# Kernel optimization log

Measured on AMD Instinct MI355X. Metric: run time of the kernel, lower is better.

Reference implementation:

```python
import jax, jax.numpy as jnp
import numpy as np

B, S, D, H, HD = 2, 1024, 1024, 16, 64
CKV, CQ, R, DFF, L, V = 256, 384, 32, 2816, 4, 32000
EPS = 1.1920929e-07  # torch RMSNorm default eps = finfo(float32).eps


def rmsnorm(x, w):
    return x * jax.lax.rsqrt(jnp.mean(x * x, -1, keepdims=True) + EPS) * w


def rope(x, base=10000.0):
    # x: [B, H, S, d]; GPT-NeoX style rotate-half, matches RoPE._neg_half
    d, s = x.shape[-1], x.shape[2]
    theta = 1.0 / base ** (jnp.arange(0, d, 2, dtype=jnp.float32) / d)
    ang = jnp.arange(s, dtype=jnp.float32)[:, None] * theta[None, :]
    ang = jnp.concatenate([ang, ang], -1)  # [s, d]
    neg = jnp.concatenate([-x[..., d // 2:], x[..., :d // 2]], -1)
    return x * jnp.cos(ang) + neg * jnp.sin(ang)


def forward(tokens, embed, w_kv_down, b_kv_down, w_q_down, b_q_down, w_kv_up, b_kv_up,
            w_q_up, b_q_up, w_o, b_o, kv_norm_w, q_norm_w, norm1_w, norm2_w,
            w_in, b_in, w_out, b_out, norm_f_w, w_head, b_head):
    h = embed[tokens]                                  # [B, S, D]
    causal = jnp.triu(jnp.ones((S, S), bool), 1)       # True above diagonal -> masked
    scale = np.float32(1.0 / np.sqrt(HD + R))
    for i in range(L):
        xn = rmsnorm(h, norm1_w[i])
        ckv = xn @ w_kv_down[i] + b_kv_down[i]         # [B, S, CKV+R]
        c_kv, k_rope = ckv[..., :CKV], ckv[..., CKV:]
        kv = rmsnorm(c_kv, kv_norm_w[i]) @ w_kv_up[i] + b_kv_up[i]
        kv = kv.reshape(B, S, H, 2 * HD).transpose(0, 2, 1, 3)  # [B, H, S, 2*HD]
        k, v = kv[..., :HD], kv[..., HD:]
        qf = rmsnorm(xn @ w_q_down[i] + b_q_down[i], q_norm_w[i]) @ w_q_up[i] + b_q_up[i]
        qf = qf.reshape(B, S, H, HD + R).transpose(0, 2, 1, 3)   # [B, H, S, HD+R]
        q, q_rope = qf[..., :HD], qf[..., HD:]
        k_rope = rope(k_rope[:, None, :, :])           # [B, 1, S, R], shared across heads
        q_rope = rope(q_rope)
        k = jnp.concatenate([k, jnp.broadcast_to(k_rope, (B, H, S, R))], -1)
        q = jnp.concatenate([q, q_rope], -1)
        a = jnp.einsum('bhqd,bhkd->bhqk', q, k) * scale
        a = jax.nn.softmax(jnp.where(causal, -jnp.inf, a), -1)
        attn = jnp.einsum('bhqk,bhkd->bhqd', a, v).transpose(0, 2, 1, 3).reshape(B, S, D)
        h = h + attn @ w_o[i] + b_o[i]
        uv = rmsnorm(h, norm2_w[i]) @ w_in[i] + b_in[i]  # [B, S, 2*DFF]
        h = h + (uv[..., :DFF] * jax.nn.silu(uv[..., DFF:])) @ w_out[i] + b_out[i]
    return rmsnorm(h, norm_f_w) @ w_head + b_head        # [B, S, V]


def setup_inputs() -> dict:
    key = jax.random.key(0)
    it = iter(jax.random.split(key, 24))
    w = lambda shp: jax.random.normal(next(it), shp, jnp.float32) * 0.02
    return dict(
        tokens=jax.random.randint(next(it), (B, S), 0, V),
        embed=w((V, D)),
        w_kv_down=w((L, D, CKV + R)), b_kv_down=w((L, CKV + R)),
        w_q_down=w((L, D, CQ)), b_q_down=w((L, CQ)),
        w_kv_up=w((L, CKV, 2 * HD * H)), b_kv_up=w((L, 2 * HD * H)),
        w_q_up=w((L, CQ, (HD + R) * H)), b_q_up=w((L, (HD + R) * H)),
        w_o=w((L, D, D)), b_o=w((L, D)),
        kv_norm_w=jnp.ones((L, CKV)), q_norm_w=jnp.ones((L, CQ)),
        norm1_w=jnp.ones((L, D)), norm2_w=jnp.ones((L, D)),
        w_in=w((L, D, 2 * DFF)), b_in=w((L, 2 * DFF)),
        w_out=w((L, DFF, D)), b_out=w((L, D)),
        norm_f_w=jnp.ones((D,)),
        w_head=w((D, V)), b_head=w((V,)),
    )


def reference(tokens, embed, w_kv_down, b_kv_down, w_q_down, b_q_down, w_kv_up, b_kv_up,
              w_q_up, b_q_up, w_o, b_o, kv_norm_w, q_norm_w, norm1_w, norm2_w,
              w_in, b_in, w_out, b_out, norm_f_w, w_head, b_head):
    return forward(tokens, embed, w_kv_down, b_kv_down, w_q_down, b_q_down, w_kv_up,
                   b_kv_up, w_q_up, b_q_up, w_o, b_o, kv_norm_w, q_norm_w, norm1_w,
                   norm2_w, w_in, b_in, w_out, b_out, norm_f_w, w_head, b_head)
```

## Files before the change

kernel.cpp:

```cpp
#include <hip/hip_runtime.h>
#include <cstdint>
#include <cstddef>

typedef unsigned short u16;
typedef __attribute__((__ext_vector_type__(8))) __bf16 bf16x8;
typedef __attribute__((__ext_vector_type__(4))) float f32x4;
typedef __attribute__((__ext_vector_type__(8))) unsigned short u16x8;

#define DEVI __device__ __forceinline__

constexpr int Bb = 2, Ss = 1024, Dd = 1024, Hh = 16;
constexpr int Mm = Bb * Ss;
constexpr int QKD = 128;
constexpr float EPSF = 1.1920929e-07f;
constexpr float NEG = -1e30f;
constexpr float QSCALE = 0.10206207261596577f;
constexpr float LOG1E4_16 = 9.210340371976184f / 16.f;

DEVI u16 f2b(float f) {
  union { float f; uint32_t u; } a; a.f = f;
  uint32_t r = a.u + 0x7FFFu + ((a.u >> 16) & 1u);
  return (u16)(r >> 16);
}
DEVI float b2f(u16 h) {
  union { uint32_t u; float f; } a; a.u = ((uint32_t)h) << 16; return a.f;
}

struct WJob { const float* src; u16* dst; long src_lstride; int K; int N; int perm; int ntiles; };
struct WJobs { WJob j[7]; };

__global__ __launch_bounds__(256) void k_wcvt_batch(WJobs jobs, int njobs,
                                                    int tiles_per_layer, long dst_lstride) {
  int bt = blockIdx.x;
  int layer = bt / tiles_per_layer;
  int t = bt - layer * tiles_per_layer;
  int ji = 0;
  while (ji < njobs - 1 && t >= jobs.j[ji].ntiles) { t -= jobs.j[ji].ntiles; ++ji; }
  const float* __restrict__ src = jobs.j[ji].src + (size_t)layer * jobs.j[ji].src_lstride;
  u16* __restrict__ dst = jobs.j[ji].dst + (size_t)layer * dst_lstride;
  const int K = jobs.j[ji].K, N = jobs.j[ji].N, perm = jobs.j[ji].perm;
  const int ktiles = K >> 6;
  const int bk = (t % ktiles) * 64;
  const int bn = (t / ktiles) * 64;
  __shared__ float ts[64][65];
  const int tid = threadIdx.x;
  {
    int c4 = tid & 15, r = tid >> 4;
    #pragma unroll
    for (int p = 0; p < 4; ++p) {
      int row = r + p * 16;
      int col = bn + c4 * 4;
      float4 v = make_float4(0.f, 0.f, 0.f, 0.f);
      if (col < N) v = *(const float4*)(src + (size_t)(bk + row) * N + col);
      ts[row][c4 * 4 + 0] = v.x; ts[row][c4 * 4 + 1] = v.y;
      ts[row][c4 * 4 + 2] = v.z; ts[row][c4 * 4 + 3] = v.w;
    }
  }
  __syncthreads();
  {
    int k8 = tid & 7, c = tid >> 3;
    #pragma unroll
    for (int p = 0; p < 2; ++p) {
      int cc = c + p * 32;
      int gcol = bn + cc;
      int row = perm ? ((gcol < 2816) ? (gcol * 2) : ((gcol - 2816) * 2 + 1)) : gcol;
      u16x8 o;
      #pragma unroll
      for (int q = 0; q < 8; ++q) o[q] = f2b(ts[k8 * 8 + q][cc]);
      *(u16x8*)(dst + (size_t)row * K + bk + k8 * 8) = o;
    }
  }
}

__global__ void k_embed(const int* __restrict__ tok, const float* __restrict__ emb,
                        float* __restrict__ h) {
  int m = blockIdx.x;
  int t = tok[m];
  const float4* src = (const float4*)(emb + (size_t)t * Dd);
  float4* dst = (float4*)(h + (size_t)m * Dd);
  dst[threadIdx.x] = src[threadIdx.x];
}

__global__ void k_rms(const float* __restrict__ in, int inStride,
                      const float* __restrict__ w, u16* __restrict__ out, int K) {
  int m = blockIdx.x;
  const float* x = in + (size_t)m * inStride;
  float ss = 0.f;
  for (int i = threadIdx.x; i < K; i += 256) { float v = x[i]; ss += v * v; }
  #pragma unroll
  for (int off = 32; off; off >>= 1) ss += __shfl_xor(ss, off);
  __shared__ float red[4];
  if ((threadIdx.x & 63) == 0) red[threadIdx.x >> 6] = ss;
  __syncthreads();
  float r = rsqrtf((red[0] + red[1] + red[2] + red[3]) / (float)K + EPSF);
  for (int i = threadIdx.x; i < K; i += 256)
    out[(size_t)m * K + i] = f2b(x[i] * r * w[i]);
}

__global__ void k_rms2(const float* __restrict__ in, const float* __restrict__ w1,
                       const float* __restrict__ w2, u16* __restrict__ out1,
                       u16* __restrict__ out2) {
  int m = blockIdx.x;
  const float* x = in + (size_t)m * 768;
  int tid = threadIdx.x;
  __shared__ float red[4];
  {
    float v = x[tid];
    float ss = v * v;
    #pragma unroll
    for (int off = 32; off; off >>= 1) ss += __shfl_xor(ss, off);
    if ((tid & 63) == 0) red[tid >> 6] = ss;
    __syncthreads();
    float r = rsqrtf((red[0] + red[1] + red[2] + red[3]) / 256.f + EPSF);
    out1[(size_t)m * 256 + tid] = f2b(v * r * w1[tid]);
    __syncthreads();
  }
  {
    float v0 = x[384 + tid];
    float v1 = (tid < 128) ? x[640 + tid] : 0.f;
    float ss = v0 * v0 + v1 * v1;
    #pragma unroll
    for (int off = 32; off; off >>= 1) ss += __shfl_xor(ss, off);
    if ((tid & 63) == 0) red[tid >> 6] = ss;
    __syncthreads();
    float r = rsqrtf((red[0] + red[1] + red[2] + red[3]) / 384.f + EPSF);
    out2[(size_t)m * 384 + tid] = f2b(v0 * r * w2[tid]);
    if (tid < 128) out2[(size_t)m * 384 + 256 + tid] = f2b(v1 * r * w2[256 + tid]);
  }
}

__global__ void k_buildkv(const u16* __restrict__ kv, const float* __restrict__ ckvq,
                          u16* __restrict__ Kb, u16* __restrict__ Vt) {
  int bh = blockIdx.x, chunk = blockIdx.y, role = blockIdx.z;
  int b = bh >> 4, h = bh & 15;
  if (role < 2) {
    __shared__ u16 t[32][33];
    int tx = threadIdx.x & 31, ty = threadIdx.x >> 5;
    int s0 = chunk * 32, d0 = role * 32;
    #pragma unroll
    for (int i = ty; i < 32; i += 8)
      t[i][tx] = kv[(size_t)(b * Ss + s0 + i) * 2048 + h * 128 + 64 + d0 + tx];
    __syncthreads();
    #pragma unroll
    for (int i = ty; i < 32; i += 8)
      Vt[((size_t)bh * 64 + d0 + i) * Ss + s0 + tx] = t[tx][i];
  } else {
    int idx = threadIdx.x;
    int d = idx & 127, r0 = idx >> 7;
    #pragma unroll
    for (int it = 0; it < 16; ++it) {
      int s = chunk * 32 + it * 2 + r0;
      int m = b * Ss + s;
      u16 kvv = 0;
      if (d < 64) kvv = kv[(size_t)m * 2048 + h * 128 + d];
      else if (d < 96) {
        int j = d - 64;
        float theta = __expf(-(float)(j & 15) * LOG1E4_16);
        float sn, cs;
        __sincosf((float)s * theta, &sn, &cs);
        const float* rr = ckvq + (size_t)m * 768 + 256;
        float x = rr[j], o = rr[j ^ 16];
        kvv = f2b(x * cs + ((j < 16) ? -o : o) * sn);
      }
      Kb[((size_t)bh * Ss + s) * QKD + d] = kvv;
    }
  }
}

#define GAS __attribute__((address_space(1)))
#define LAS __attribute__((address_space(3)))
DEVI void gll16(const void* g, void* l) {
  __builtin_amdgcn_global_load_lds((GAS const void*)g, (LAS void*)l, 16, 0, 0);
}
#define VMW(n) asm volatile("s_waitcnt vmcnt(" #n ")" ::: "memory")
#define FENCE asm volatile("" ::: "memory")

__global__ __launch_bounds__(256) void k_flash(
    const u16* __restrict__ qf, const u16* __restrict__ Kg,
    const u16* __restrict__ Vtg, u16* __restrict__ attn) {
  __shared__ u16 lK[2][64 * 128];
  __shared__ u16 lV[2][64 * 64];
  __shared__ u16 lP[4][16 * 64];
  const int tid = threadIdx.x;
  const int pair = blockIdx.x, bh = blockIdx.y;
  const int b = bh >> 4, h = bh & 15;
  const int lane = tid & 63, w = tid >> 6;
  const int g = lane >> 4, fr = lane & 15;
  const u16* Kh = Kg + (size_t)bh * Ss * QKD;
  const u16* Vh = Vtg + (size_t)bh * 64 * Ss;

  auto stageKV = [&](int buf, int kt) {
    int r = tid >> 4, c = tid & 15;
    #pragma unroll
    for (int gg = 0; gg < 4; ++gg) {
      int row = gg * 16 + r;
      const u16* src = Kh + (size_t)(kt * 64 + row) * QKD + ((c ^ (row & 7)) * 8);
      gll16(src, (u16*)lK[buf] + gg * 2048 + tid * 8);
    }
    int r2 = tid >> 3, c2 = tid & 7;
    #pragma unroll
    for (int gg = 0; gg < 2; ++gg) {
      int d = gg * 32 + r2;
      const u16* src = Vh + (size_t)d * Ss + kt * 64 + ((c2 ^ (d & 7)) * 8);
      gll16(src, (u16*)lV[buf] + gg * 2048 + tid * 8);
    }
  };

  for (int pass = 0; pass < 2; ++pass) {
    const int qt = pass ? (15 - pair) : pair;
    const int q0 = qt * 64;
    const int s_row = q0 + w * 16 + fr;
    const u16* qrow = qf + (size_t)(b * Ss + s_row) * 1536 + h * 96;
    bf16x8 af[4];
    {
      u16x8 r0 = *(const u16x8*)(qrow + g * 8);
      u16x8 r1 = *(const u16x8*)(qrow + 32 + g * 8);
      u16x8 r2 = *(const u16x8*)(qrow + 64 + g * 8);
      u16x8 a0, a1, a2, a3;
      #pragma unroll
      for (int q = 0; q < 8; ++q) {
        a0[q] = f2b(b2f(r0[q]) * QSCALE);
        a1[q] = f2b(b2f(r1[q]) * QSCALE);
        float x = b2f(r2[q]);
        float oth = __shfl_xor(x, 32);
        int jj = (g & 1) * 8 + q;
        float theta = __expf(-(float)jj * LOG1E4_16);
        float sn, cs;
        __sincosf((float)s_row * theta, &sn, &cs);
        float v = x * cs + ((g < 2) ? -oth : oth) * sn;
        a2[q] = f2b(v * QSCALE);
        a3[q] = 0;
      }
      af[0] = *(bf16x8*)&a0; af[1] = *(bf16x8*)&a1;
      af[2] = *(bf16x8*)&a2; af[3] = *(bf16x8*)&a3;
    }

    f32x4 acc_o[4] = {};
    float mrow = NEG, lrow = 0.f;

    stageKV(0, 0);

    for (int kt = 0; kt <= qt; ++kt) {
      const int cur = kt & 1;
      if (kt < qt) { stageKV(cur ^ 1, kt + 1); VMW(6); }
      else { VMW(0); }
      __builtin_amdgcn_s_barrier();
      FENCE;

      f32x4 accs[4] = {};
      #pragma unroll
      for (int j = 0; j < 4; ++j) {
        #pragma unroll
        for (int k4 = 0; k4 < 4; ++k4) {
          int row = j * 16 + fr;
          int ch = (k4 * 4 + g) ^ (row & 7);
          bf16x8 kf = *(const bf16x8*)&lK[cur][row * 128 + ch * 8];
          accs[j] = __builtin_amdgcn_mfma_f32_16x16x32_bf16(kf, af[k4], accs[j], 0, 0, 0);
        }
      }

      float p[16];
      float tmax = NEG;
      #pragma unroll
      for (int j = 0; j < 4; ++j)
        #pragma unroll
        for (int r = 0; r < 4; ++r) {
          float s = accs[j][r];
          int kloc = j * 16 + 4 * g + r;
          bool valid = (kt < qt) || (kloc <= w * 16 + fr);
          s = valid ? s : NEG;
          p[j * 4 + r] = s;
          tmax = fmaxf(tmax, s);
        }
      tmax = fmaxf(tmax, __shfl_xor(tmax, 16));
      tmax = fmaxf(tmax, __shfl_xor(tmax, 32));
      float mnew = fmaxf(mrow, tmax);
      float scale = __expf(mrow - mnew);
      float tsum = 0.f;
      #pragma unroll
      for (int i = 0; i < 16; ++i) { p[i] = __expf(p[i] - mnew); tsum += p[i]; }
      tsum += __shfl_xor(tsum, 16);
      tsum += __shfl_xor(tsum, 32);
      lrow = lrow * scale + tsum;
      mrow = mnew;

      #pragma unroll
      for (int j = 0; j < 4; ++j)
        #pragma unroll
        for (int t = 0; t < 2; ++t) {
          uint32_t u = (uint32_t)f2b(p[j * 4 + 2 * t]) |
                       ((uint32_t)f2b(p[j * 4 + 2 * t + 1]) << 16);
          int kp = 8 * j + 2 * g + t;
          int ch = kp >> 2, wi = kp & 3;
          ((uint32_t*)lP[w])[fr * 32 + ((ch ^ (fr & 7)) << 2) + wi] = u;
        }

      float sc_q[4];
      #pragma unroll
      for (int r = 0; r < 4; ++r) sc_q[r] = __shfl(scale, 4 * g + r);
      #pragma unroll
      for (int j2 = 0; j2 < 4; ++j2)
        #pragma unroll
        for (int r = 0; r < 4; ++r) acc_o[j2][r] *= sc_q[r];

      #pragma unroll
      for (int ksub = 0; ksub < 2; ++ksub) {
        int chp = (4 * ksub + g) ^ (fr & 7);
        bf16x8 pa = *(const bf16x8*)&((const u16*)lP[w])[fr * 64 + chp * 8];
        #pragma unroll
        for (int j2 = 0; j2 < 4; ++j2) {
          int d = j2 * 16 + fr;
          int chv = (ksub * 4 + g) ^ (d & 7);
          bf16x8 vf = *(const bf16x8*)&lV[cur][d * 64 + chv * 8];
          acc_o[j2] = __builtin_amdgcn_mfma_f32_16x16x32_bf16(pa, vf, acc_o[j2], 0, 0, 0);
        }
      }
      FENCE;
      __builtin_amdgcn_s_barrier();
      FENCE;
    }

    float li[4];
    #pragma unroll
    for (int r = 0; r < 4; ++r) li[r] = 1.f / __shfl(lrow, 4 * g + r);
    #pragma unroll
    for (int j2 = 0; j2 < 4; ++j2)
      #pragma unroll
      for (int r = 0; r < 4; ++r) {
        int q = q0 + w * 16 + 4 * g + r;
        int d = j2 * 16 + fr;
        attn[((size_t)(b * Ss) + q) * Dd + h * 64 + d] = f2b(acc_o[j2][r] * li[r]);
      }
  }
}

template <int MODE, int BM, int BN>
DEVI void gemm_core(const u16* __restrict__ A, const u16* __restrict__ Bt,
                    const float* __restrict__ bias, const float* __restrict__ bias2,
                    void* __restrict__ C, int N, int K, int bx, int by,
                    u16* lA, u16* lB) {
  constexpr int MI = BM / 32, NJ = BN / 32;
  constexpr int AL = BM / 64, BL = BN / 64;
  constexpr int ASZ = BM * 32, BSZ = BN * 32;
  const int tid = threadIdx.x;
  const long m0 = (long)bx * BM, n0 = (long)by * BN;
  const int lane = tid & 63, wid = tid >> 6;
  const int wm = (wid >> 1) * (BM / 2), wn = (wid & 1) * (BN / 2);
  const int fr = lane & 15, l4 = lane >> 4;
  const int sw = (fr >> 1) & 3;

  const int rs = tid >> 2;
  const int cs = ((tid & 3) ^ ((rs >> 1) & 3)) * 8;
  const u16* a0 = A + (m0 + rs) * (long)K + cs;
  const u16* b0 = Bt + (n0 + rs) * (long)K + cs;
  const long g64 = 64L * K;

  f32x4 acc[MI][NJ] = {};
  const int NT = K >> 5;

  auto stage = [&](int buf, int kk) {
    #pragma unroll
    for (int g = 0; g < AL; ++g)
      gll16(a0 + g * g64 + kk, lA + buf * ASZ + g * 2048 + tid * 8);
    #pragma unroll
    for (int g = 0; g < BL; ++g)
      gll16(b0 + g * g64 + kk, lB + buf * BSZ + g * 2048 + tid * 8);
  };

  stage(0, 0);

  for (int j = 0; j < NT; ++j) {
    const int cur = j & 1;
    const int kk1 = (j + 1) << 5;
    if (j + 1 < NT) {
      stage(cur ^ 1, kk1);
      if constexpr (AL + BL == 2) VMW(2);
      else if constexpr (AL + BL == 3) VMW(3);
      else if constexpr (AL + BL == 4) VMW(4);
      else if constexpr (AL + BL == 5) VMW(5);
      else VMW(6);
    } else {
      VMW(0);
    }
    __builtin_amdgcn_s_barrier();
    FENCE;
    bf16x8 af[MI], bfr[NJ];
    #pragma unroll
    for (int i = 0; i < MI; i++)
      af[i] = *(const bf16x8*)&lA[cur * ASZ + (wm + i * 16 + fr) * 32 + ((l4 ^ sw) * 8)];
    #pragma unroll
    for (int jj = 0; jj < NJ; jj++)
      bfr[jj] = *(const bf16x8*)&lB[cur * BSZ + (wn + jj * 16 + fr) * 32 + ((l4 ^ sw) * 8)];
    #pragma unroll
    for (int i = 0; i < MI; i++)
      #pragma unroll
      for (int jj = 0; jj < NJ; jj++)
        acc[i][jj] = __builtin_amdgcn_mfma_f32_16x16x32_bf16(af[i], bfr[jj], acc[i][jj], 0, 0, 0);
    FENCE;
    __builtin_amdgcn_s_barrier();
    FENCE;
  }

  const long r0 = m0 + wm + l4 * 4;
  const long c0 = n0 + wn + fr;
  if (MODE == 3) {
    u16* G = (u16*)C;
    #pragma unroll
    for (int j = 0; j < NJ; ++j) {
      long col = c0 + j * 16;
      int pcol = (int)((col & 1) ? (col >> 1) + 2816 : (col >> 1));
      float bs = bias[pcol];
      #pragma unroll
      for (int i = 0; i < MI; ++i)
        #pragma unroll
        for (int r = 0; r < 4; ++r) {
          float val = acc[i][j][r] + bs;
          float oth = __shfl_xor(val, 1);
          if (!(col & 1)) {
            float x = oth;
            float gv = val * x * (1.f / (1.f + __expf(-x)));
            G[(r0 + i * 16 + r) * 2816L + (col >> 1)] = f2b(gv);
          }
        }
    }
  } else {
    #pragma unroll
    for (int j = 0; j < NJ; ++j) {
      long col = c0 + j * 16;
      float bs;
      if (MODE == 4)
        bs = (col < 288) ? bias[col] : ((col >= 384) ? bias2[col - 384] : 0.f);
      else
        bs = bias[col];
      #pragma unroll
      for (int i = 0; i < MI; ++i)
        #pragma unroll
        for (int r = 0; r < 4; ++r) {
          long row = r0 + i * 16 + r;
          float val = acc[i][j][r] + bs;
          if (MODE == 0 || MODE == 4) ((float*)C)[row * N + col] = val;
          else if (MODE == 1) { float* p = (float*)C + row * N + col; *p += val; }
          else ((u16*)C)[row * N + col] = f2b(val);
        }
    }
  }
}

template <int MODE, int BM, int BN, int MINW = 4>
__global__ __launch_bounds__(256, MINW) void k_gemm(
    const u16* __restrict__ A, const u16* __restrict__ Bt,
    const float* __restrict__ bias, const float* __restrict__ bias2,
    void* __restrict__ C, int N, int K) {
  __shared__ u16 lA[2 * BM * 32];
  __shared__ u16 lB[2 * BN * 32];
  const int gx = gridDim.x;
  const int nwg = gx * gridDim.y;
  const int f = blockIdx.y * gx + blockIdx.x;
  const int f2 = (f & 7) * (nwg >> 3) + (f >> 3);
  const int bx = f2 % gx, by = f2 / gx;
  gemm_core<MODE, BM, BN>(A, Bt, bias, bias2, C, N, K, bx, by, lA, lB);
}

__global__ __launch_bounds__(256, 4) void k_gemm_pair(
    const u16* A0, const u16* Bt0, const float* b0, void* C0, int N0, int K0, int gy0,
    const u16* A1, const u16* Bt1, const float* b1, void* C1, int N1, int K1, int gy1) {
  __shared__ u16 lA[2 * 64 * 32];
  __shared__ u16 lB[2 * 128 * 32];
  const int z = blockIdx.z;
  const int gy = z ? gy1 : gy0;
  if ((int)blockIdx.y >= gy) return;
  const int gx = gridDim.x;
  const int nwg = gx * gy;
  const int f = blockIdx.y * gx + blockIdx.x;
  const int f2 = (f & 7) * (nwg >> 3) + (f >> 3);
  const int bx = f2 % gx, by = f2 / gx;
  if (z) gemm_core<2, 64, 128>(A1, Bt1, b1, nullptr, C1, N1, K1, bx, by, lA, lB);
  else   gemm_core<2, 64, 128>(A0, Bt0, b0, nullptr, C0, N0, K0, bx, by, lA, lB);
}

extern "C" void kernel_launch(void* const* d_in, const int* in_sizes, int n_in,
                              void* d_out, int out_size, void* d_ws, size_t ws_size,
                              hipStream_t stream) {
  (void)in_sizes; (void)n_in; (void)out_size; (void)ws_size;
  const int*   tokens    = (const int*)  d_in[0];
  const float* embed     = (const float*)d_in[1];
  const float* w_kv_down = (const float*)d_in[2];
  const float* b_kv_down = (const float*)d_in[3];
  const float* w_q_down  = (const float*)d_in[4];
  const float* b_q_down  = (const float*)d_in[5];
  const float* w_kv_up   = (const float*)d_in[6];
  const float* b_kv_up   = (const float*)d_in[7];
  const float* w_q_up    = (const float*)d_in[8];
  const float* b_q_up    = (const float*)d_in[9];
  const float* w_o       = (const float*)d_in[10];
  const float* b_o       = (const float*)d_in[11];
  const float* kv_norm_w = (const float*)d_in[12];
  const float* q_norm_w  = (const float*)d_in[13];
  const float* norm1_w   = (const float*)d_in[14];
  const float* norm2_w   = (const float*)d_in[15];
  const float* w_in      = (const float*)d_in[16];
  const float* b_in      = (const float*)d_in[17];
  const float* w_out     = (const float*)d_in[18];
  const float* b_out     = (const float*)d_in[19];
  const float* norm_f_w  = (const float*)d_in[20];
  const float* w_head    = (const float*)d_in[21];
  const float* b_head    = (const float*)d_in[22];

  char* base = (char*)d_ws;
  size_t off = 0;
  auto alloc = [&](size_t bytes) -> void* {
    void* p = base + off;
    off += (bytes + 255) & ~(size_t)255;
    return p;
  };
  const long O_DQ = 0, O_KVUP = 786432, O_QUP = 1310720, O_O = 1900544,
             O_IN = 2949120, O_OUT = 8716288, LSLOT = 11599872;
  u16* warena = (u16*)alloc((size_t)4 * LSLOT * 2);

  float* h     = (float*)alloc((size_t)Mm * 1024 * 4);
  u16*   xn    = (u16*)  alloc((size_t)Mm * 1024 * 2);
  float* ckvq  = (float*)alloc((size_t)Mm * 768 * 4);
  u16*   ckvn  = (u16*)  alloc((size_t)Mm * 256 * 2);
  u16*   kv    = (u16*)  alloc((size_t)Mm * 2048 * 2);
  u16*   qdn   = (u16*)  alloc((size_t)Mm * 384 * 2);
  u16*   qf    = (u16*)  alloc((size_t)Mm * 1536 * 2);
  u16*   Kb    = (u16*)  alloc((size_t)32 * 1024 * QKD * 2);
  u16*   Vt    = (u16*)  alloc((size_t)32 * 64 * 1024 * 2);
  u16*   attn  = (u16*)  alloc((size_t)Mm * 1024 * 2);
  u16*   gate  = (u16*)  alloc((size_t)Mm * 2816 * 2);

  k_embed<<<Mm, 256, 0, stream>>>(tokens, embed, h);

  {
    WJobs jb;
    jb.j[0] = { w_kv_down, warena + O_DQ,              1024L * 288,  1024, 288,  0, 96 };
    jb.j[1] = { w_q_down,  warena + O_DQ + 384 * 1024, 1024L * 384,  1024, 384,  0, 96 };
    jb.j[2] = { w_kv_up,   warena + O_KVUP,            256L * 2048,  256,  2048, 0, 128 };
    jb.j[3] = { w_q_up,    warena + O_QUP,             384L * 1536,  384,  1536, 0, 144 };
    jb.j[4] = { w_o,       warena + O_O,               1024L * 1024, 1024, 1024, 0, 256 };
    jb.j[5] = { w_in,      warena + O_IN,              1024L * 5632, 1024, 5632, 1, 1408 };
    jb.j[6] = { w_out,     warena + O_OUT,             2816L * 1024, 2816, 1024, 0, 704 };
    k_wcvt_batch<<<4 * 2832, 256, 0, stream>>>(jb, 7, 2832, LSLOT);
  }

  for (int l = 0; l < 4; l++) {
    u16* wl = warena + (size_t)l * LSLOT;
    u16* wT_dq  = wl + O_DQ;
    u16* wT_kvup = wl + O_KVUP;
    u16* wT_qup = wl + O_QUP;
    u16* wT_o   = wl + O_O;
    u16* wT_in  = wl + O_IN;
    u16* wT_out = wl + O_OUT;

    k_rms<<<Mm, 256, 0, stream>>>(h, 1024, norm1_w + l * 1024, xn, 1024);
    k_gemm<4, 64, 64><<<dim3(32, 12), 256, 0, stream>>>(xn, wT_dq, b_kv_down + l * 288,
                                                        b_q_down + l * 384, ckvq, 768, 1024);
    k_rms2<<<Mm, 256, 0, stream>>>(ckvq, kv_norm_w + l * 256, q_norm_w + l * 384,
                                   ckvn, qdn);
    k_gemm_pair<<<dim3(32, 16, 2), 256, 0, stream>>>(
        ckvn, wT_kvup, b_kv_up + l * 2048, kv, 2048, 256, 16,
        qdn,  wT_qup,  b_q_up + l * 1536,  qf, 1536, 384, 12);
    k_buildkv<<<dim3(32, 32, 3), 256, 0, stream>>>(kv, ckvq, Kb, Vt);
    k_flash<<<dim3(8, 32), 256, 0, stream>>>(qf, Kb, Vt, attn);
    k_gemm<1, 64, 64><<<dim3(32, 16), 256, 0, stream>>>(attn, wT_o, b_o + l * 1024,
                                                        nullptr, h, 1024, 1024);
    k_rms<<<Mm, 256, 0, stream>>>(h, 1024, norm2_w + l * 1024, xn, 1024);
    k_gemm<3, 128, 128><<<dim3(16, 44), 256, 0, stream>>>(xn, wT_in, b_in + l * 5632,
                                                          nullptr, gate, 5632, 1024);
    k_gemm<1, 64, 64><<<dim3(32, 16), 256, 0, stream>>>(gate, wT_out, b_out + l * 1024,
                                                        nullptr, h, 1024, 2816);
  }

  k_rms<<<Mm, 256, 0, stream>>>(h, 1024, norm_f_w, xn, 1024);
  {
    WJobs jbh;
    jbh.j[0] = { w_head, warena, 0, 1024, 32000, 0, 8000 };
    k_wcvt_batch<<<8000, 256, 0, stream>>>(jbh, 1, 8000, 0);
  }
  k_gemm<0, 128, 128><<<dim3(16, 250), 256, 0, stream>>>(xn, warena, b_head,
                                                         nullptr, (float*)d_out, 32000, 1024);
}
```

Before: 986.0 us.

## Triple-buffer GEMM LDS staging and fold head weight conversion into batch kernel

The GEMM main loop moves from double to triple buffering in LDS, issuing loads two k-steps ahead and adjusting the vmcnt waits to match. This is meant to hide more global-load latency. The LM-head weight conversion now runs in the initial batched conversion launch, writing to its own workspace buffer instead of reusing the layer arena, which removes one kernel launch. The cost is 1.5x the LDS per block, which can lower occupancy for the 128x128 tiles, plus an extra 64MB of workspace.

```diff
diff --git a/kernel.cpp b/kernel.cpp
--- a/kernel.cpp
+++ b/kernel.cpp
@@ -30,15 +30,23 @@
 struct WJobs { WJob j[7]; };
 
 __global__ __launch_bounds__(256) void k_wcvt_batch(WJobs jobs, int njobs,
-                                                    int tiles_per_layer, long dst_lstride) {
+                                                    int tiles_per_layer, long dst_lstride,
+                                                    int ltot, const float* hsrc, u16* hdst) {
   int bt = blockIdx.x;
-  int layer = bt / tiles_per_layer;
-  int t = bt - layer * tiles_per_layer;
-  int ji = 0;
-  while (ji < njobs - 1 && t >= jobs.j[ji].ntiles) { t -= jobs.j[ji].ntiles; ++ji; }
-  const float* __restrict__ src = jobs.j[ji].src + (size_t)layer * jobs.j[ji].src_lstride;
-  u16* __restrict__ dst = jobs.j[ji].dst + (size_t)layer * dst_lstride;
-  const int K = jobs.j[ji].K, N = jobs.j[ji].N, perm = jobs.j[ji].perm;
+  const float* __restrict__ src;
+  u16* __restrict__ dst;
+  int K, N, perm, t;
+  if (bt >= ltot) {
+    t = bt - ltot; src = hsrc; dst = hdst; K = 1024; N = 32000; perm = 0;
+  } else {
+    int layer = bt / tiles_per_layer;
+    t = bt - layer * tiles_per_layer;
+    int ji = 0;
+    while (ji < njobs - 1 && t >= jobs.j[ji].ntiles) { t -= jobs.j[ji].ntiles; ++ji; }
+    src = jobs.j[ji].src + (size_t)layer * jobs.j[ji].src_lstride;
+    dst = jobs.j[ji].dst + (size_t)layer * dst_lstride;
+    K = jobs.j[ji].K; N = jobs.j[ji].N; perm = jobs.j[ji].perm;
+  }
   const int ktiles = K >> 6;
   const int bk = (t % ktiles) * 64;
   const int bn = (t / ktiles) * 64;
@@ -368,17 +376,20 @@
   };
 
   stage(0, 0);
-
+  stage(1, 32);
+
+  int cur = 0;
   for (int j = 0; j < NT; ++j) {
-    const int cur = j & 1;
-    const int kk1 = (j + 1) << 5;
-    if (j + 1 < NT) {
-      stage(cur ^ 1, kk1);
+    if (j + 2 < NT) {
+      int nxt2 = (cur >= 1) ? cur - 1 : 2;
+      stage(nxt2, (j + 2) << 5);
+      if constexpr (AL + BL == 2) VMW(4);
+      else if constexpr (AL + BL == 3) VMW(6);
+      else VMW(8);
+    } else if (j + 1 < NT) {
       if constexpr (AL + BL == 2) VMW(2);
       else if constexpr (AL + BL == 3) VMW(3);
-      else if constexpr (AL + BL == 4) VMW(4);
-      else if constexpr (AL + BL == 5) VMW(5);
-      else VMW(6);
+      else VMW(4);
     } else {
       VMW(0);
     }
@@ -399,6 +410,7 @@
     FENCE;
     __builtin_amdgcn_s_barrier();
     FENCE;
+    cur = (cur == 2) ? 0 : cur + 1;
   }
 
   const long r0 = m0 + wm + l4 * 4;
@@ -451,8 +463,8 @@
     const u16* __restrict__ A, const u16* __restrict__ Bt,
     const float* __restrict__ bias, const float* __restrict__ bias2,
     void* __restrict__ C, int N, int K) {
-  __shared__ u16 lA[2 * BM * 32];
-  __shared__ u16 lB[2 * BN * 32];
+  __shared__ u16 lA[3 * BM * 32];
+  __shared__ u16 lB[3 * BN * 32];
   const int gx = gridDim.x;
   const int nwg = gx * gridDim.y;
   const int f = blockIdx.y * gx + blockIdx.x;
@@ -464,8 +476,8 @@
 __global__ __launch_bounds__(256, 4) void k_gemm_pair(
     const u16* A0, const u16* Bt0, const float* b0, void* C0, int N0, int K0, int gy0,
     const u16* A1, const u16* Bt1, const float* b1, void* C1, int N1, int K1, int gy1) {
-  __shared__ u16 lA[2 * 64 * 32];
-  __shared__ u16 lB[2 * 128 * 32];
+  __shared__ u16 lA[3 * 64 * 32];
+  __shared__ u16 lB[3 * 128 * 32];
   const int z = blockIdx.z;
   const int gy = z ? gy1 : gy0;
   if ((int)blockIdx.y >= gy) return;
@@ -516,6 +528,7 @@
   const long O_DQ = 0, O_KVUP = 786432, O_QUP = 1310720, O_O = 1900544,
              O_IN = 2949120, O_OUT = 8716288, LSLOT = 11599872;
   u16* warena = (u16*)alloc((size_t)4 * LSLOT * 2);
+  u16* wThead = (u16*)alloc((size_t)32000 * 1024 * 2);
 
   float* h     = (float*)alloc((size_t)Mm * 1024 * 4);
   u16*   xn    = (u16*)  alloc((size_t)Mm * 1024 * 2);
@@ -540,7 +553,8 @@
     jb.j[4] = { w_o,       warena + O_O,               1024L * 1024, 1024, 1024, 0, 256 };
     jb.j[5] = { w_in,      warena + O_IN,              1024L * 5632, 1024, 5632, 1, 1408 };
     jb.j[6] = { w_out,     warena + O_OUT,             2816L * 1024, 2816, 1024, 0, 704 };
-    k_wcvt_batch<<<4 * 2832, 256, 0, stream>>>(jb, 7, 2832, LSLOT);
+    k_wcvt_batch<<<4 * 2832 + 8000, 256, 0, stream>>>(jb, 7, 2832, LSLOT,
+                                                      4 * 2832, w_head, wThead);
   }
 
   for (int l = 0; l < 4; l++) {
@@ -572,11 +586,6 @@
   }
 
   k_rms<<<Mm, 256, 0, stream>>>(h, 1024, norm_f_w, xn, 1024);
-  {
-    WJobs jbh;
-    jbh.j[0] = { w_head, warena, 0, 1024, 32000, 0, 8000 };
-    k_wcvt_batch<<<8000, 256, 0, stream>>>(jbh, 1, 8000, 0);
-  }
-  k_gemm<0, 128, 128><<<dim3(16, 250), 256, 0, stream>>>(xn, warena, b_head,
+  k_gemm<0, 128, 128><<<dim3(16, 250), 256, 0, stream>>>(xn, wThead, b_head,
                                                          nullptr, (float*)d_out, 32000, 1024);
 }
```

Result: slower. 1.163 ms (+17.9%).
